# Performance work log

Hardware: AMD Instinct MI355X
Metric: run time of the kernel (lower is better)

Reference implementation:

```python
import jax, jax.numpy as jnp
import numpy as np

NUM = 128
IN_F = NUM * NUM        # 16384
HID = NUM * 3           # 384 (infl_ratio = 3)
OUT = 10
BATCH = 8192
BN_EPS = 1e-5


def sign_ste(t):
    # Deterministic sign binarization with straight-through gradient,
    # matching the torch .data/.org mutation trick.
    return t + jax.lax.stop_gradient(jnp.sign(t) - t)


def setup_inputs() -> dict:
    key = jax.random.key(0)
    k_x, k_w1, k_w4 = jax.random.split(key, 3)
    x = jax.random.normal(k_x, (BATCH, IN_F), dtype=jnp.float32)
    W1 = jax.random.normal(k_w1, (HID, IN_F), dtype=jnp.float32) * 0.02
    W4 = jax.random.normal(k_w4, (OUT, HID), dtype=jnp.float32) * 0.02
    gamma = jnp.ones((HID,), dtype=jnp.float32)
    beta = jnp.zeros((HID,), dtype=jnp.float32)
    return {"x": x, "W1": W1, "gamma": gamma, "beta": beta, "W4": W4}


def reference(x, W1, gamma, beta, W4):
    x = x.reshape(-1, IN_F)
    # fc1: in_features (16384) != 784, so the hard-coded check binarizes the input too
    xb = sign_ste(x)
    h = jnp.einsum('bk,hk->bh', xb, sign_ste(W1))  # [B, HID]
    # BatchNorm1d, training mode: batch stats, biased variance
    mean = jnp.mean(h, axis=0)
    var = jnp.mean(jnp.square(h - mean), axis=0)
    h = (h - mean) * jax.lax.rsqrt(var + BN_EPS) * gamma + beta
    # Hardtanh
    h = jnp.clip(h, -1.0, 1.0)
    # fc4: input size 384 != 784 -> binarize activations, binarize weights
    out = jnp.einsum('bh,oh->bo', sign_ste(h), sign_ste(W4))  # [B, 10]
    return out
```

## Files before the change

kernel.cpp:

```cpp
#include <hip/hip_runtime.h>
#include <cstdint>
#include <cstddef>


typedef float v4f __attribute__((ext_vector_type(4)));
typedef long long v2l __attribute__((ext_vector_type(2)));

#define BATCH   8192
#define KDIM    16384
#define HID     384
#define OUT_F   10
#define BK      64
#define MT      32
#define SPLITK  4
#define KPB     (KDIM / SPLITK)
#define NIT     (KPB / BK)
#define WCHUNK  (HID * BK)

#define WS_W1C   0
#define WS_H     (6291456)
#define WS_GSUM  (WS_H + 12582912)
#define WS_GSQ   (WS_GSUM + 3072)
#define WS_MEAN  (WS_GSQ + 3072)
#define WS_COEF  (WS_MEAN + 3072)
#define WS_SW4   (WS_COEF + 3072)

__device__ __forceinline__ uint32_t pack_sign4(v4f v) {
    uint32_t p = 0;
#pragma unroll
    for (int i = 0; i < 4; ++i) {
        uint32_t u = __float_as_uint(v[i]);
        uint32_t b = ((u & 0x7fffffffu) == 0u) ? 0u : (0x38u | ((u >> 24) & 0x80u));
        p |= b << (8 * i);
    }
    return p;
}

__global__ void prep_w1(const float* __restrict__ W1, uint8_t* __restrict__ W1c) {
    size_t e = ((size_t)blockIdx.x * blockDim.x + threadIdx.x) * 4;
    int c   = (int)(e >> 14);
    int k   = (int)(e & 16383);
    int it  = k >> 6;
    int kin = k & 63;
    int s   = kin >> 5;
    int q   = (kin >> 3) & 3;
    int j   = kin & 7;
    v4f w = *(const v4f*)(W1 + e);
    uint32_t p = pack_sign4(w);
    *(uint32_t*)(W1c + (((size_t)it * HID + c) * 4 + q) * 16 + s * 8 + j) = p;
}

__global__ __launch_bounds__(256, 4) void gemm1(const float* __restrict__ x,
                                                const uint8_t* __restrict__ W1c,
                                                float* __restrict__ h) {
    __shared__ __align__(16) uint8_t Xs[2][MT * 72];

    const int t    = threadIdx.x;
    const int wave = t >> 6;
    const int lane = t & 63;
    const int q    = lane >> 4;
    const int l15  = lane & 15;
    const int kblk = blockIdx.x & (SPLITK - 1);
    const int m0   = (blockIdx.x >> 2) * MT;

    const int xrow = t >> 3;
    const int xk8  = (t & 7) * 8;
    const float* xp = x + (size_t)(m0 + xrow) * KDIM + (size_t)kblk * KPB + xk8;

    const uint8_t* wp = W1c + (size_t)kblk * ((size_t)NIT * WCHUNK)
                      + (((size_t)(wave * 96 + l15)) * 4 + q) * 16;

    v4f acc[2][6];
#pragma unroll
    for (int mt = 0; mt < 2; ++mt)
#pragma unroll
        for (int nt = 0; nt < 6; ++nt)
            acc[mt][nt] = v4f{0.f, 0.f, 0.f, 0.f};

    v2l wc[6];
    {
#pragma unroll
        for (int nt = 0; nt < 6; ++nt)
            wc[nt] = *(const v2l*)(wp + nt * 1024);
        v4f xa = *(const v4f*)(xp);
        v4f xb = *(const v4f*)(xp + 4);
        uint2 pk; pk.x = pack_sign4(xa); pk.y = pack_sign4(xb);
        *(uint2*)&Xs[0][xrow * 72 + xk8] = pk;
    }
    __syncthreads();

#pragma unroll 2
    for (int it = 0; it < NIT; ++it) {
        const int cur = it & 1;
        const bool more = (it + 1) < NIT;
        v2l wn[6];
        v4f xa, xb;
        if (more) {
            const uint8_t* wpn = wp + (size_t)(it + 1) * WCHUNK;
#pragma unroll
            for (int nt = 0; nt < 6; ++nt)
                wn[nt] = *(const v2l*)(wpn + nt * 1024);
            xa = *(const v4f*)(xp + (size_t)(it + 1) * BK);
            xb = *(const v4f*)(xp + (size_t)(it + 1) * BK + 4);
        }

#pragma unroll
        for (int s = 0; s < 2; ++s) {
            long long a[2];
#pragma unroll
            for (int mt = 0; mt < 2; ++mt)
                a[mt] = *(const long long*)&Xs[cur][(mt * 16 + l15) * 72 + s * 32 + q * 8];
#pragma unroll
            for (int nt = 0; nt < 6; ++nt)
#pragma unroll
                for (int mt = 0; mt < 2; ++mt)
                    acc[mt][nt] = __builtin_amdgcn_mfma_f32_16x16x32_fp8_fp8(
                        a[mt], wc[nt][s], acc[mt][nt], 0, 0, 0);
        }

        if (more) {
            uint2 pk; pk.x = pack_sign4(xa); pk.y = pack_sign4(xb);
            *(uint2*)&Xs[cur ^ 1][xrow * 72 + xk8] = pk;
#pragma unroll
            for (int nt = 0; nt < 6; ++nt) wc[nt] = wn[nt];
        }
        __syncthreads();
    }

#pragma unroll
    for (int nt = 0; nt < 6; ++nt) {
        const int col = wave * 96 + nt * 16 + l15;
#pragma unroll
        for (int mt = 0; mt < 2; ++mt)
#pragma unroll
            for (int r = 0; r < 4; ++r)
                atomicAdd(&h[(size_t)(m0 + mt * 16 + q * 4 + r) * HID + col],
                          acc[mt][nt][r]);
    }
}

__global__ void colstats(const float* __restrict__ h,
                         double* __restrict__ gsum, double* __restrict__ gsq) {
    int j  = threadIdx.x;
    int r0 = blockIdx.x * 16;
    double s = 0.0, sq = 0.0;
#pragma unroll
    for (int r = 0; r < 16; ++r) {
        double v = (double)h[(size_t)(r0 + r) * HID + j];
        s += v;
        sq += v * v;
    }
    atomicAdd(&gsum[j], s);
    atomicAdd(&gsq[j], sq);
}

__global__ void finalize(const double* __restrict__ gsum, const double* __restrict__ gsq,
                         const float* __restrict__ gamma, const float* __restrict__ W4,
                         double* __restrict__ meanArr, double* __restrict__ coefArr,
                         float* __restrict__ sW4) {
    int j = threadIdx.x;
    double mean = gsum[j] * (1.0 / (double)BATCH);
    double var  = gsq[j] * (1.0 / (double)BATCH) - mean * mean;
    meanArr[j] = mean;
    coefArr[j] = (double)gamma[j] / sqrt(var + 1e-5);
#pragma unroll
    for (int o = 0; o < OUT_F; ++o) {
        float w = W4[o * HID + j];
        sW4[o * HID + j] = (w > 0.f) ? 1.f : ((w < 0.f) ? -1.f : 0.f);
    }
}

__global__ __launch_bounds__(256) void head(const float* __restrict__ h,
                                            const double* __restrict__ meanArr,
                                            const double* __restrict__ coefArr,
                                            const float* __restrict__ beta,
                                            const float* __restrict__ sW4,
                                            float* __restrict__ out) {
    int wave = threadIdx.x >> 6;
    int lane = threadIdx.x & 63;
    int b = blockIdx.x * 4 + wave;
    float a[OUT_F];
#pragma unroll
    for (int o = 0; o < OUT_F; ++o) a[o] = 0.f;
#pragma unroll
    for (int i = 0; i < 6; ++i) {
        int j = lane + i * 64;
        double v = ((double)h[(size_t)b * HID + j] - meanArr[j]) * coefArr[j]
                 + (double)beta[j];
        float s = (v > 0.0) ? 1.f : ((v < 0.0) ? -1.f : 0.f);
#pragma unroll
        for (int o = 0; o < OUT_F; ++o) a[o] += s * sW4[o * HID + j];
    }
#pragma unroll
    for (int o = 0; o < OUT_F; ++o) {
#pragma unroll
        for (int off = 32; off > 0; off >>= 1) a[o] += __shfl_down(a[o], off);
    }
    if (lane == 0) {
#pragma unroll
        for (int o = 0; o < OUT_F; ++o) out[(size_t)b * OUT_F + o] = a[o];
    }
}

extern "C" void kernel_launch(void* const* d_in, const int* in_sizes, int n_in,
                              void* d_out, int out_size, void* d_ws, size_t ws_size,
                              hipStream_t stream) {
    const float* x     = (const float*)d_in[0];
    const float* W1    = (const float*)d_in[1];
    const float* gamma = (const float*)d_in[2];
    const float* beta  = (const float*)d_in[3];
    const float* W4    = (const float*)d_in[4];
    float* out = (float*)d_out;

    uint8_t* ws = (uint8_t*)d_ws;
    uint8_t* W1c     = ws + WS_W1C;
    float*   h       = (float*)(ws + WS_H);
    double*  gsum    = (double*)(ws + WS_GSUM);
    double*  gsq     = (double*)(ws + WS_GSQ);
    double*  meanArr = (double*)(ws + WS_MEAN);
    double*  coefArr = (double*)(ws + WS_COEF);
    float*   sW4     = (float*)(ws + WS_SW4);

    prep_w1<<<6144, 256, 0, stream>>>(W1, W1c);
    hipMemsetAsync(ws + WS_H, 0, 12582912 + 2 * HID * sizeof(double), stream);
    gemm1<<<(BATCH / MT) * SPLITK, 256, 0, stream>>>(x, W1c, h);
    colstats<<<BATCH / 16, HID, 0, stream>>>(h, gsum, gsq);
    finalize<<<1, HID, 0, stream>>>(gsum, gsq, gamma, W4, meanArr, coefArr, sW4);
    head<<<BATCH / 4, 256, 0, stream>>>(h, meanArr, coefArr, beta, sW4, out);
}
```

Measured before the change: 795.3 us.

## Pre-binarize x to fp8, drop LDS staging, replace split-K atomics with partial buffers

Adds a prep_x pass that converts the fp32 input to packed fp8 sign bytes once. gemm1 then loads A fragments straight from global memory into registers, with no LDS double buffer and no __syncthreads. Split-K results go to four separate partial buffers with plain stores instead of float atomics into h, and colstats sums those partials while computing the column statistics, so the large memset is no longer needed. The cost is an extra full pass over x (read fp32, write fp8) and about 50MB of extra partial-buffer traffic, in exchange for lighter gemm inner loops and no atomic contention.

```diff
diff --git a/kernel.cpp b/kernel.cpp
--- a/kernel.cpp
+++ b/kernel.cpp
@@ -18,8 +18,10 @@
 #define WCHUNK  (HID * BK)
 
 #define WS_W1C   0
-#define WS_H     (6291456)
-#define WS_GSUM  (WS_H + 12582912)
+#define WS_X8    6291456
+#define WS_HP    140509184
+#define WS_H     190840832
+#define WS_GSUM  203423744
 #define WS_GSQ   (WS_GSUM + 3072)
 #define WS_MEAN  (WS_GSQ + 3072)
 #define WS_COEF  (WS_MEAN + 3072)
@@ -34,6 +36,16 @@
         p |= b << (8 * i);
     }
     return p;
+}
+
+__global__ void prep_x(const float* __restrict__ x, uint8_t* __restrict__ x8) {
+    size_t e = ((size_t)blockIdx.x * blockDim.x + threadIdx.x) * 16;
+    uint4 p;
+    p.x = pack_sign4(*(const v4f*)(x + e));
+    p.y = pack_sign4(*(const v4f*)(x + e + 4));
+    p.z = pack_sign4(*(const v4f*)(x + e + 8));
+    p.w = pack_sign4(*(const v4f*)(x + e + 12));
+    *(uint4*)(x8 + e) = p;
 }
 
 __global__ void prep_w1(const float* __restrict__ W1, uint8_t* __restrict__ W1c) {
@@ -50,11 +62,9 @@
     *(uint32_t*)(W1c + (((size_t)it * HID + c) * 4 + q) * 16 + s * 8 + j) = p;
 }
 
-__global__ __launch_bounds__(256, 4) void gemm1(const float* __restrict__ x,
+__global__ __launch_bounds__(256, 4) void gemm1(const uint8_t* __restrict__ x8,
                                                 const uint8_t* __restrict__ W1c,
-                                                float* __restrict__ h) {
-    __shared__ __align__(16) uint8_t Xs[2][MT * 72];
-
+                                                float* __restrict__ hpart) {
     const int t    = threadIdx.x;
     const int wave = t >> 6;
     const int lane = t & 63;
@@ -63,10 +73,7 @@
     const int kblk = blockIdx.x & (SPLITK - 1);
     const int m0   = (blockIdx.x >> 2) * MT;
 
-    const int xrow = t >> 3;
-    const int xk8  = (t & 7) * 8;
-    const float* xp = x + (size_t)(m0 + xrow) * KDIM + (size_t)kblk * KPB + xk8;
-
+    const uint8_t* xq = x8 + (size_t)(m0 + l15) * KDIM + (size_t)kblk * KPB + q * 8;
     const uint8_t* wp = W1c + (size_t)kblk * ((size_t)NIT * WCHUNK)
                       + (((size_t)(wave * 96 + l15)) * 4 + q) * 16;
 
@@ -77,56 +84,46 @@
         for (int nt = 0; nt < 6; ++nt)
             acc[mt][nt] = v4f{0.f, 0.f, 0.f, 0.f};
 
-    v2l wc[6];
-    {
-#pragma unroll
-        for (int nt = 0; nt < 6; ++nt)
-            wc[nt] = *(const v2l*)(wp + nt * 1024);
-        v4f xa = *(const v4f*)(xp);
-        v4f xb = *(const v4f*)(xp + 4);
-        uint2 pk; pk.x = pack_sign4(xa); pk.y = pack_sign4(xb);
-        *(uint2*)&Xs[0][xrow * 72 + xk8] = pk;
-    }
-    __syncthreads();
+    long long ac[2][2];
+#pragma unroll
+    for (int mt = 0; mt < 2; ++mt)
+#pragma unroll
+        for (int s = 0; s < 2; ++s)
+            ac[mt][s] = *(const long long*)(xq + (size_t)mt * 16 * KDIM + s * 32);
 
 #pragma unroll 2
     for (int it = 0; it < NIT; ++it) {
-        const int cur = it & 1;
-        const bool more = (it + 1) < NIT;
-        v2l wn[6];
-        v4f xa, xb;
-        if (more) {
-            const uint8_t* wpn = wp + (size_t)(it + 1) * WCHUNK;
-#pragma unroll
-            for (int nt = 0; nt < 6; ++nt)
-                wn[nt] = *(const v2l*)(wpn + nt * 1024);
-            xa = *(const v4f*)(xp + (size_t)(it + 1) * BK);
-            xb = *(const v4f*)(xp + (size_t)(it + 1) * BK + 4);
-        }
-
-#pragma unroll
-        for (int s = 0; s < 2; ++s) {
-            long long a[2];
-#pragma unroll
-            for (int mt = 0; mt < 2; ++mt)
-                a[mt] = *(const long long*)&Xs[cur][(mt * 16 + l15) * 72 + s * 32 + q * 8];
+        v2l w[6];
+        const uint8_t* wi = wp + (size_t)it * WCHUNK;
+#pragma unroll
+        for (int nt = 0; nt < 6; ++nt)
+            w[nt] = *(const v2l*)(wi + nt * 1024);
+
+        long long an[2][2];
+        const uint8_t* xi = xq + (size_t)(it + 1) * BK;
+#pragma unroll
+        for (int mt = 0; mt < 2; ++mt)
+#pragma unroll
+            for (int s = 0; s < 2; ++s)
+                an[mt][s] = *(const long long*)(xi + (size_t)mt * 16 * KDIM + s * 32);
+
+#pragma unroll
+        for (int s = 0; s < 2; ++s)
 #pragma unroll
             for (int nt = 0; nt < 6; ++nt)
 #pragma unroll
                 for (int mt = 0; mt < 2; ++mt)
                     acc[mt][nt] = __builtin_amdgcn_mfma_f32_16x16x32_fp8_fp8(
-                        a[mt], wc[nt][s], acc[mt][nt], 0, 0, 0);
-        }
-
-        if (more) {
-            uint2 pk; pk.x = pack_sign4(xa); pk.y = pack_sign4(xb);
-            *(uint2*)&Xs[cur ^ 1][xrow * 72 + xk8] = pk;
-#pragma unroll
-            for (int nt = 0; nt < 6; ++nt) wc[nt] = wn[nt];
-        }
-        __syncthreads();
-    }
-
+                        ac[mt][s], w[nt][s], acc[mt][nt], 0, 0, 0);
+
+#pragma unroll
+        for (int mt = 0; mt < 2; ++mt)
+#pragma unroll
+            for (int s = 0; s < 2; ++s)
+                ac[mt][s] = an[mt][s];
+    }
+
+    float* hp = hpart + (size_t)kblk * BATCH * HID;
 #pragma unroll
     for (int nt = 0; nt < 6; ++nt) {
         const int col = wave * 96 + nt * 16 + l15;
@@ -134,21 +131,25 @@
         for (int mt = 0; mt < 2; ++mt)
 #pragma unroll
             for (int r = 0; r < 4; ++r)
-                atomicAdd(&h[(size_t)(m0 + mt * 16 + q * 4 + r) * HID + col],
-                          acc[mt][nt][r]);
-    }
-}
-
-__global__ void colstats(const float* __restrict__ h,
+                hp[(size_t)(m0 + mt * 16 + q * 4 + r) * HID + col] = acc[mt][nt][r];
+    }
+}
+
+__global__ void colstats(const float* __restrict__ hpart, float* __restrict__ h,
                          double* __restrict__ gsum, double* __restrict__ gsq) {
     int j  = threadIdx.x;
-    int r0 = blockIdx.x * 16;
+    int r0 = blockIdx.x * 32;
     double s = 0.0, sq = 0.0;
-#pragma unroll
-    for (int r = 0; r < 16; ++r) {
-        double v = (double)h[(size_t)(r0 + r) * HID + j];
-        s += v;
-        sq += v * v;
+#pragma unroll 4
+    for (int r = 0; r < 32; ++r) {
+        size_t idx = (size_t)(r0 + r) * HID + j;
+        float v = hpart[idx] + hpart[idx + (size_t)1 * BATCH * HID]
+                + hpart[idx + (size_t)2 * BATCH * HID]
+                + hpart[idx + (size_t)3 * BATCH * HID];
+        h[idx] = v;
+        double d = (double)v;
+        s += d;
+        sq += d * d;
     }
     atomicAdd(&gsum[j], s);
     atomicAdd(&gsq[j], sq);
@@ -214,6 +215,8 @@
 
     uint8_t* ws = (uint8_t*)d_ws;
     uint8_t* W1c     = ws + WS_W1C;
+    uint8_t* x8      = ws + WS_X8;
+    float*   hpart   = (float*)(ws + WS_HP);
     float*   h       = (float*)(ws + WS_H);
     double*  gsum    = (double*)(ws + WS_GSUM);
     double*  gsq     = (double*)(ws + WS_GSQ);
@@ -222,9 +225,10 @@
     float*   sW4     = (float*)(ws + WS_SW4);
 
     prep_w1<<<6144, 256, 0, stream>>>(W1, W1c);
-    hipMemsetAsync(ws + WS_H, 0, 12582912 + 2 * HID * sizeof(double), stream);
-    gemm1<<<(BATCH / MT) * SPLITK, 256, 0, stream>>>(x, W1c, h);
-    colstats<<<BATCH / 16, HID, 0, stream>>>(h, gsum, gsq);
+    prep_x<<<(BATCH * (size_t)KDIM) / 16 / 256, 256, 0, stream>>>(x, x8);
+    hipMemsetAsync(gsum, 0, 2 * HID * sizeof(double), stream);
+    gemm1<<<(BATCH / MT) * SPLITK, 256, 0, stream>>>(x8, W1c, hpart);
+    colstats<<<BATCH / 32, HID, 0, stream>>>(hpart, h, gsum, gsq);
     finalize<<<1, HID, 0, stream>>>(gsum, gsq, gamma, W4, meanArr, coefArr, sW4);
     head<<<BATCH / 4, 256, 0, stream>>>(h, meanArr, coefArr, beta, sW4, out);
 }
```

Measured after the change: 951.8 us. 19.7% more time.
